# Optimization experiments

Hardware: AMD Instinct MI355X
Metric: run time of the kernel (lower is better)

The kernel has to match this reference:

```python
import jax, jax.numpy as jnp
import numpy as np

B, N, T, H = 64, 16, 128, 256  # batch, max_neighbors, time_steps, hidden_dim


def setup_inputs() -> dict:
    key = jax.random.key(0)
    ks = jax.random.split(key, 7)
    inv_h = 1.0 / np.sqrt(H)
    return {
        "node_rnn_output": jax.random.normal(ks[0], (B, T, H), jnp.float32),
        "neigh_rnn_output": jax.random.normal(ks[1], (B, N, T, H), jnp.float32),
        "neighbors_number": N,
        "Wq": jax.random.normal(ks[2], (H, H), jnp.float32) * inv_h,
        "Wk": jax.random.normal(ks[3], (H, H), jnp.float32) * inv_h,
        "Wv": jax.random.normal(ks[4], (H, H), jnp.float32) * inv_h,
        "Wb": jax.random.normal(ks[5], (H, H), jnp.float32) * inv_h,
        "b": jnp.zeros((T,), jnp.float32),
    }


def reference(node_rnn_output, neigh_rnn_output, neighbors_number, Wq, Wk, Wv, Wb, b):
    # key_values: node prepended to neighbors -> [B, N+1, T, H]
    kv = jnp.concatenate((node_rnn_output[:, None], neigh_rnn_output), axis=1)
    # torch nn.Linear: x @ W^T
    q = node_rnn_output @ Wq.T            # [B, T, H] (query is identical across neighbor slots)
    key = kv @ Wk.T                       # [B, N+1, T, H]
    value = kv @ Wv.T                     # [B, N+1, T, H]
    # bilinear score: (q @ Wb) @ key^T + b  (b broadcasts over last axis)
    qW = q @ Wb                           # [B, T, H]
    S = jnp.einsum('bth,bnsh->bnts', qW, key) + b  # [B, N+1, T, T]
    A = jax.nn.softmax(S, axis=-1)        # dropout is identity at eval / drop_prob=0
    outputs = jnp.einsum('bnts,bnsh->bnth', A, value)  # [B, N+1, T, H]
    return outputs, A
```

## Files before the change

### kernel.cpp

```cpp
#include <hip/hip_runtime.h>
#include <cstdio>


typedef __bf16 bf16;
typedef __attribute__((ext_vector_type(8))) __bf16 bf16x8;
typedef __attribute__((ext_vector_type(4))) __bf16 bf16x4;
typedef __attribute__((ext_vector_type(4))) float floatx4;

#define MFMA_BF16 __builtin_amdgcn_mfma_f32_16x16x32_bf16

__device__ __forceinline__ const float* kv_row_ptr(const float* node, const float* neigh, int bn, int s) {
  int b = bn / 17, nn = bn % 17;
  return (nn == 0) ? node + ((size_t)b * 128 + s) * 256
                   : neigh + (((size_t)b * 16 + (nn - 1)) * 128 + s) * 256;
}

__global__ __launch_bounds__(256) void k_wc(const float* __restrict__ Wq, const float* __restrict__ Wb,
                                            float* __restrict__ Wc) {
  int m = blockIdx.x, h = threadIdx.x;
  float acc = 0.f;
  for (int k = 0; k < 256; ++k) acc = fmaf(Wq[k * 256 + m], Wb[k * 256 + h], acc);
  Wc[m * 256 + h] = acc;
}

__global__ __launch_bounds__(256) void k_we(const float* __restrict__ Wc, const float* __restrict__ Wk,
                                            float* __restrict__ We) {
  int m = blockIdx.x, g = threadIdx.x;
  float acc = 0.f;
  for (int k = 0; k < 256; ++k) acc = fmaf(Wc[m * 256 + k], Wk[k * 256 + g], acc);
  We[m * 256 + g] = acc;
}

__global__ __launch_bounds__(256) void k_wvb(const float* __restrict__ Wv, bf16* __restrict__ Wvb) {
  int i = (blockIdx.x * 256 + threadIdx.x) * 4;
  float4 v = *(const float4*)(Wv + i);
  bf16x4 o;
  o[0] = (bf16)v.x; o[1] = (bf16)v.y; o[2] = (bf16)v.z; o[3] = (bf16)v.w;
  *(bf16x4*)(Wvb + i) = o;
}

__global__ __launch_bounds__(256) void k_qwk(const float* __restrict__ X, const float* __restrict__ W,
                                             float* __restrict__ Y) {
  __shared__ float As[32][64];
  __shared__ float Bs[32][64];
  int tid = threadIdx.x;
  int m0 = blockIdx.x * 64, n0 = blockIdx.y * 64;
  int tx = tid & 15, ty = tid >> 4;
  float acc[4][4] = {};
  int r = tid >> 3, c4 = (tid & 7) * 4;
  int kr = tid >> 4, c4b = (tid & 15) * 4;
  for (int k0 = 0; k0 < 256; k0 += 32) {
#pragma unroll
    for (int p = 0; p < 2; ++p) {
      float4 v = *(const float4*)(X + (size_t)(m0 + r + p * 32) * 256 + k0 + c4);
      As[c4 + 0][r + p * 32] = v.x; As[c4 + 1][r + p * 32] = v.y;
      As[c4 + 2][r + p * 32] = v.z; As[c4 + 3][r + p * 32] = v.w;
    }
#pragma unroll
    for (int p = 0; p < 2; ++p) {
      float4 v = *(const float4*)(W + (size_t)(k0 + kr + p * 16) * 256 + n0 + c4b);
      *(float4*)&Bs[kr + p * 16][c4b] = v;
    }
    __syncthreads();
#pragma unroll 8
    for (int k = 0; k < 32; ++k) {
      float a[4], bb[4];
#pragma unroll
      for (int i = 0; i < 4; ++i) a[i] = As[k][ty * 4 + i];
#pragma unroll
      for (int j = 0; j < 4; ++j) bb[j] = Bs[k][tx * 4 + j];
#pragma unroll
      for (int i = 0; i < 4; ++i)
#pragma unroll
        for (int j = 0; j < 4; ++j) acc[i][j] = fmaf(a[i], bb[j], acc[i][j]);
    }
    __syncthreads();
  }
#pragma unroll
  for (int i = 0; i < 4; ++i) {
    float4 v = make_float4(acc[i][0], acc[i][1], acc[i][2], acc[i][3]);
    *(float4*)(Y + (size_t)(m0 + ty * 4 + i) * 256 + n0 + tx * 4) = v;
  }
}

#define QKS 40
#define ABS 136
__global__ __launch_bounds__(256) void k_fused(const float* __restrict__ qWk, const float* __restrict__ node,
                                               const float* __restrict__ neigh, const float* __restrict__ bvec,
                                               const bf16* __restrict__ Wvb,
                                               float* __restrict__ Aout, float* __restrict__ Out) {
  __shared__ __align__(16) char smem[52224];
  bf16* Khi = (bf16*)smem;
  bf16* Klo = (bf16*)(smem + 10240);
  bf16* Ab  = (bf16*)smem;
  bf16* Vt  = (bf16*)(smem + 34816);

  int tid = threadIdx.x;
  int w = tid >> 6, lane = tid & 63, lrow = lane & 15, quad = lane >> 4;
  int bn = blockIdx.x;
  const float* Q = qWk + (size_t)(bn / 17) * 128 * 256;
  const float* K = kv_row_ptr(node, neigh, bn, 0);

  int srow = tid >> 1;
  int skb = (tid & 1) * 16;

  floatx4 acc[2][8];
#pragma unroll
  for (int rt = 0; rt < 2; ++rt)
#pragma unroll
    for (int ct = 0; ct < 8; ++ct) acc[rt][ct] = (floatx4)0.0f;

  const float* kb = K + (size_t)srow * 256 + skb;
  const float* qlane = Q + (size_t)(w * 32 + lrow) * 256 + quad * 8;
  float4 pk[4];
#pragma unroll
  for (int j = 0; j < 4; ++j) pk[j] = *(const float4*)(kb + j * 4);

  for (int k0 = 0; k0 < 256; k0 += 32) {
#pragma unroll
    for (int half = 0; half < 2; ++half) {
      float kf[8] = {pk[half * 2].x, pk[half * 2].y, pk[half * 2].z, pk[half * 2].w,
                     pk[half * 2 + 1].x, pk[half * 2 + 1].y, pk[half * 2 + 1].z, pk[half * 2 + 1].w};
      bf16x8 kh, kl;
#pragma unroll
      for (int u = 0; u < 8; ++u) {
        bf16 h2 = (bf16)kf[u]; kh[u] = h2; kl[u] = (bf16)(kf[u] - (float)h2);
      }
      int off = srow * QKS + skb + half * 8;
      *(bf16x8*)&Khi[off] = kh; *(bf16x8*)&Klo[off] = kl;
    }
    if (k0 < 224) {
#pragma unroll
      for (int j = 0; j < 4; ++j) pk[j] = *(const float4*)(kb + k0 + 32 + j * 4);
    }
    float4 q0[2], q1[2];
#pragma unroll
    for (int rt = 0; rt < 2; ++rt) {
      const float* qp = qlane + (size_t)rt * 16 * 256 + k0;
      q0[rt] = *(const float4*)qp;
      q1[rt] = *(const float4*)(qp + 4);
    }
    __syncthreads();
    bf16x8 ah[2], al[2];
#pragma unroll
    for (int rt = 0; rt < 2; ++rt) {
      float qf[8] = {q0[rt].x, q0[rt].y, q0[rt].z, q0[rt].w,
                     q1[rt].x, q1[rt].y, q1[rt].z, q1[rt].w};
#pragma unroll
      for (int u = 0; u < 8; ++u) {
        bf16 h = (bf16)qf[u]; ah[rt][u] = h; al[rt][u] = (bf16)(qf[u] - (float)h);
      }
    }
#pragma unroll
    for (int ct = 0; ct < 8; ++ct) {
      int off = (ct * 16 + lrow) * QKS + quad * 8;
      bf16x8 bh = *(const bf16x8*)&Khi[off];
      bf16x8 bl = *(const bf16x8*)&Klo[off];
#pragma unroll
      for (int rt = 0; rt < 2; ++rt) {
        acc[rt][ct] = MFMA_BF16(ah[rt], bh, acc[rt][ct], 0, 0, 0);
        acc[rt][ct] = MFMA_BF16(al[rt], bh, acc[rt][ct], 0, 0, 0);
        acc[rt][ct] = MFMA_BF16(ah[rt], bl, acc[rt][ct], 0, 0, 0);
      }
    }
    __syncthreads();
  }

  float bvv[8];
#pragma unroll
  for (int ct = 0; ct < 8; ++ct) bvv[ct] = bvec[ct * 16 + lrow];
#pragma unroll
  for (int rt = 0; rt < 2; ++rt)
#pragma unroll
    for (int r = 0; r < 4; ++r) {
      float mx = -3.402823466e+38f;
#pragma unroll
      for (int ct = 0; ct < 8; ++ct) {
        float v = acc[rt][ct][r] + bvv[ct];
        acc[rt][ct][r] = v;
        mx = fmaxf(mx, v);
      }
#pragma unroll
      for (int off = 1; off < 16; off <<= 1) mx = fmaxf(mx, __shfl_xor(mx, off, 64));
      float s = 0.f;
#pragma unroll
      for (int ct = 0; ct < 8; ++ct) {
        float e = __expf(acc[rt][ct][r] - mx);
        acc[rt][ct][r] = e;
        s += e;
      }
#pragma unroll
      for (int off = 1; off < 16; off <<= 1) s += __shfl_xor(s, off, 64);
      float inv = 1.f / s;
#pragma unroll
      for (int ct = 0; ct < 8; ++ct) acc[rt][ct][r] *= inv;
    }

  float* Ag = Aout + (size_t)bn * 128 * 128;
#pragma unroll
  for (int rt = 0; rt < 2; ++rt)
#pragma unroll
    for (int r = 0; r < 4; ++r) {
      int row = w * 32 + rt * 16 + quad * 4 + r;
#pragma unroll
      for (int ct = 0; ct < 8; ++ct) {
        int s = ct * 16 + lrow;
        float v = acc[rt][ct][r];
        Ag[(size_t)row * 128 + s] = v;
        Ab[row * ABS + s] = (bf16)v;
      }
    }

  float* Ob = Out + (size_t)bn * 128 * 256;
  for (int hh = 0; hh < 2; ++hh) {
    const int H0 = hh * 128;
    floatx4 vacc[2][8];
#pragma unroll
    for (int rt = 0; rt < 2; ++rt)
#pragma unroll
      for (int ct = 0; ct < 8; ++ct) vacc[rt][ct] = (floatx4)0.0f;

#pragma unroll
    for (int kk = 0; kk < 8; ++kk) {
      bf16x8 af[2];
#pragma unroll
      for (int rt = 0; rt < 2; ++rt) {
        const float* kp = K + (size_t)(w * 32 + rt * 16 + lrow) * 256 + kk * 32 + quad * 8;
        float4 a = *(const float4*)kp, b2 = *(const float4*)(kp + 4);
        bf16x8 o;
        o[0] = (bf16)a.x;  o[1] = (bf16)a.y;  o[2] = (bf16)a.z;  o[3] = (bf16)a.w;
        o[4] = (bf16)b2.x; o[5] = (bf16)b2.y; o[6] = (bf16)b2.z; o[7] = (bf16)b2.w;
        af[rt] = o;
      }
#pragma unroll
      for (int ct = 0; ct < 8; ++ct) {
        bf16x8 bwv = *(const bf16x8*)&Wvb[(size_t)(H0 + ct * 16 + lrow) * 256 + kk * 32 + quad * 8];
#pragma unroll
        for (int rt = 0; rt < 2; ++rt)
          vacc[rt][ct] = MFMA_BF16(af[rt], bwv, vacc[rt][ct], 0, 0, 0);
      }
    }

#pragma unroll
    for (int hc = 0; hc < 2; ++hc) {
#pragma unroll
      for (int ct = 0; ct < 4; ++ct)
#pragma unroll
        for (int rt = 0; rt < 2; ++rt) {
          bf16x4 o;
#pragma unroll
          for (int r = 0; r < 4; ++r) o[r] = (bf16)vacc[rt][hc * 4 + ct][r];
          *(bf16x4*)&Vt[(ct * 16 + lrow) * ABS + w * 32 + rt * 16 + quad * 4] = o;
        }
      __syncthreads();
      floatx4 pacc[2][4];
#pragma unroll
      for (int rt = 0; rt < 2; ++rt)
#pragma unroll
        for (int ct = 0; ct < 4; ++ct) pacc[rt][ct] = (floatx4)0.0f;
#pragma unroll
      for (int s0 = 0; s0 < 128; s0 += 32) {
        bf16x8 paf[2];
#pragma unroll
        for (int rt = 0; rt < 2; ++rt)
          paf[rt] = *(const bf16x8*)&Ab[(w * 32 + rt * 16 + lrow) * ABS + s0 + quad * 8];
#pragma unroll
        for (int ct = 0; ct < 4; ++ct) {
          bf16x8 bv8 = *(const bf16x8*)&Vt[(ct * 16 + lrow) * ABS + s0 + quad * 8];
#pragma unroll
          for (int rt = 0; rt < 2; ++rt)
            pacc[rt][ct] = MFMA_BF16(paf[rt], bv8, pacc[rt][ct], 0, 0, 0);
        }
      }
#pragma unroll
      for (int rt = 0; rt < 2; ++rt)
#pragma unroll
        for (int ct = 0; ct < 4; ++ct)
#pragma unroll
          for (int r = 0; r < 4; ++r) {
            int row = w * 32 + rt * 16 + quad * 4 + r;
            Ob[(size_t)row * 256 + H0 + hc * 64 + ct * 16 + lrow] = pacc[rt][ct][r];
          }
      __syncthreads();
    }
  }
}

extern "C" void kernel_launch(void* const* d_in, const int* in_sizes, int n_in,
                              void* d_out, int out_size, void* d_ws, size_t ws_size,
                              hipStream_t stream) {
  const float* node  = (const float*)d_in[0];
  const float* neigh = (const float*)d_in[1];
  const float* Wq = (const float*)d_in[3];
  const float* Wk = (const float*)d_in[4];
  const float* Wv = (const float*)d_in[5];
  const float* Wb = (const float*)d_in[6];
  const float* bv = (const float*)d_in[7];

  float* out  = (float*)d_out;
  float* Aout = out + (size_t)64 * 17 * 128 * 256;

  size_t need = (size_t)(65536 + 65536 + 2097152) * 4 + (size_t)65536 * 2;
  if (ws_size < need) { fprintf(stderr, "ws too small: %zu < %zu\n", ws_size, need); return; }
  float* wsf = (float*)d_ws;
  float* Wc  = wsf;
  float* We  = wsf + 65536;
  float* qWk = wsf + 131072;
  bf16*  Wvb = (bf16*)(wsf + 131072 + 2097152);

  k_wvb<<<64, 256, 0, stream>>>(Wv, Wvb);
  k_wc<<<256, 256, 0, stream>>>(Wq, Wb, Wc);
  k_we<<<256, 256, 0, stream>>>(Wc, Wk, We);
  k_qwk<<<dim3(128, 4), 256, 0, stream>>>(node, We, qWk);
  k_fused<<<1088, 256, 0, stream>>>(qWk, node, neigh, bv, Wvb, Aout, out);
}
```

Baseline: 495.0 us.

## Use 512-thread blocks in fused attention and tile weight-combination GEMMs

New measurement: 604.2 us. 1.22x slower.

```diff
diff --git a/kernel.cpp b/kernel.cpp
--- a/kernel.cpp
+++ b/kernel.cpp
@@ -13,22 +13,6 @@
   int b = bn / 17, nn = bn % 17;
   return (nn == 0) ? node + ((size_t)b * 128 + s) * 256
                    : neigh + (((size_t)b * 16 + (nn - 1)) * 128 + s) * 256;
-}
-
-__global__ __launch_bounds__(256) void k_wc(const float* __restrict__ Wq, const float* __restrict__ Wb,
-                                            float* __restrict__ Wc) {
-  int m = blockIdx.x, h = threadIdx.x;
-  float acc = 0.f;
-  for (int k = 0; k < 256; ++k) acc = fmaf(Wq[k * 256 + m], Wb[k * 256 + h], acc);
-  Wc[m * 256 + h] = acc;
-}
-
-__global__ __launch_bounds__(256) void k_we(const float* __restrict__ Wc, const float* __restrict__ Wk,
-                                            float* __restrict__ We) {
-  int m = blockIdx.x, g = threadIdx.x;
-  float acc = 0.f;
-  for (int k = 0; k < 256; ++k) acc = fmaf(Wc[m * 256 + k], Wk[k * 256 + g], acc);
-  We[m * 256 + g] = acc;
 }
 
 __global__ __launch_bounds__(256) void k_wvb(const float* __restrict__ Wv, bf16* __restrict__ Wvb) {
@@ -37,6 +21,45 @@
   bf16x4 o;
   o[0] = (bf16)v.x; o[1] = (bf16)v.y; o[2] = (bf16)v.z; o[3] = (bf16)v.w;
   *(bf16x4*)(Wvb + i) = o;
+}
+
+__global__ __launch_bounds__(256) void k_atb(const float* __restrict__ A, const float* __restrict__ B,
+                                             float* __restrict__ C) {
+  __shared__ float As[32][64];
+  __shared__ float Bs[32][64];
+  int tid = threadIdx.x;
+  int m0 = blockIdx.x * 64, n0 = blockIdx.y * 64;
+  int tx = tid & 15, ty = tid >> 4;
+  float acc[4][4] = {};
+  int kr = tid >> 4, c4 = (tid & 15) * 4;
+  for (int k0 = 0; k0 < 256; k0 += 32) {
+#pragma unroll
+    for (int p = 0; p < 2; ++p) {
+      float4 va = *(const float4*)(A + (size_t)(k0 + kr + p * 16) * 256 + m0 + c4);
+      *(float4*)&As[kr + p * 16][c4] = va;
+      float4 vb = *(const float4*)(B + (size_t)(k0 + kr + p * 16) * 256 + n0 + c4);
+      *(float4*)&Bs[kr + p * 16][c4] = vb;
+    }
+    __syncthreads();
+#pragma unroll 8
+    for (int k = 0; k < 32; ++k) {
+      float a[4], bb[4];
+#pragma unroll
+      for (int i = 0; i < 4; ++i) a[i] = As[k][ty * 4 + i];
+#pragma unroll
+      for (int j = 0; j < 4; ++j) bb[j] = Bs[k][tx * 4 + j];
+#pragma unroll
+      for (int i = 0; i < 4; ++i)
+#pragma unroll
+        for (int j = 0; j < 4; ++j) acc[i][j] = fmaf(a[i], bb[j], acc[i][j]);
+    }
+    __syncthreads();
+  }
+#pragma unroll
+  for (int i = 0; i < 4; ++i) {
+    float4 v = make_float4(acc[i][0], acc[i][1], acc[i][2], acc[i][3]);
+    *(float4*)(C + (size_t)(m0 + ty * 4 + i) * 256 + n0 + tx * 4) = v;
+  }
 }
 
 __global__ __launch_bounds__(256) void k_qwk(const float* __restrict__ X, const float* __restrict__ W,
@@ -85,10 +108,10 @@
 
 #define QKS 40
 #define ABS 136
-__global__ __launch_bounds__(256) void k_fused(const float* __restrict__ qWk, const float* __restrict__ node,
-                                               const float* __restrict__ neigh, const float* __restrict__ bvec,
-                                               const bf16* __restrict__ Wvb,
-                                               float* __restrict__ Aout, float* __restrict__ Out) {
+__global__ __launch_bounds__(512, 4) void k_fused(const float* __restrict__ qWk, const float* __restrict__ node,
+                                                  const float* __restrict__ neigh, const float* __restrict__ bvec,
+                                                  const bf16* __restrict__ Wvb,
+                                                  float* __restrict__ Aout, float* __restrict__ Out) {
   __shared__ __align__(16) char smem[52224];
   bf16* Khi = (bf16*)smem;
   bf16* Klo = (bf16*)(smem + 10240);
@@ -101,54 +124,43 @@
   const float* Q = qWk + (size_t)(bn / 17) * 128 * 256;
   const float* K = kv_row_ptr(node, neigh, bn, 0);
 
-  int srow = tid >> 1;
-  int skb = (tid & 1) * 16;
-
-  floatx4 acc[2][8];
-#pragma unroll
-  for (int rt = 0; rt < 2; ++rt)
-#pragma unroll
-    for (int ct = 0; ct < 8; ++ct) acc[rt][ct] = (floatx4)0.0f;
+  int srow = tid >> 2;
+  int skb = (tid & 3) * 8;
+
+  floatx4 acc[8];
+#pragma unroll
+  for (int ct = 0; ct < 8; ++ct) acc[ct] = (floatx4)0.0f;
 
   const float* kb = K + (size_t)srow * 256 + skb;
-  const float* qlane = Q + (size_t)(w * 32 + lrow) * 256 + quad * 8;
-  float4 pk[4];
-#pragma unroll
-  for (int j = 0; j < 4; ++j) pk[j] = *(const float4*)(kb + j * 4);
+  const float* qlane = Q + (size_t)(w * 16 + lrow) * 256 + quad * 8;
+  float4 pk[2];
+#pragma unroll
+  for (int j = 0; j < 2; ++j) pk[j] = *(const float4*)(kb + j * 4);
 
   for (int k0 = 0; k0 < 256; k0 += 32) {
-#pragma unroll
-    for (int half = 0; half < 2; ++half) {
-      float kf[8] = {pk[half * 2].x, pk[half * 2].y, pk[half * 2].z, pk[half * 2].w,
-                     pk[half * 2 + 1].x, pk[half * 2 + 1].y, pk[half * 2 + 1].z, pk[half * 2 + 1].w};
+    {
+      float kf[8] = {pk[0].x, pk[0].y, pk[0].z, pk[0].w, pk[1].x, pk[1].y, pk[1].z, pk[1].w};
       bf16x8 kh, kl;
 #pragma unroll
       for (int u = 0; u < 8; ++u) {
         bf16 h2 = (bf16)kf[u]; kh[u] = h2; kl[u] = (bf16)(kf[u] - (float)h2);
       }
-      int off = srow * QKS + skb + half * 8;
+      int off = srow * QKS + skb;
       *(bf16x8*)&Khi[off] = kh; *(bf16x8*)&Klo[off] = kl;
     }
     if (k0 < 224) {
 #pragma unroll
-      for (int j = 0; j < 4; ++j) pk[j] = *(const float4*)(kb + k0 + 32 + j * 4);
-    }
-    float4 q0[2], q1[2];
-#pragma unroll
-    for (int rt = 0; rt < 2; ++rt) {
-      const float* qp = qlane + (size_t)rt * 16 * 256 + k0;
-      q0[rt] = *(const float4*)qp;
-      q1[rt] = *(const float4*)(qp + 4);
-    }
-    __syncthreads();
-    bf16x8 ah[2], al[2];
-#pragma unroll
-    for (int rt = 0; rt < 2; ++rt) {
-      float qf[8] = {q0[rt].x, q0[rt].y, q0[rt].z, q0[rt].w,
-                     q1[rt].x, q1[rt].y, q1[rt].z, q1[rt].w};
+      for (int j = 0; j < 2; ++j) pk[j] = *(const float4*)(kb + k0 + 32 + j * 4);
+    }
+    float4 q0 = *(const float4*)(qlane + k0);
+    float4 q1 = *(const float4*)(qlane + k0 + 4);
+    __syncthreads();
+    bf16x8 ah, al;
+    {
+      float qf[8] = {q0.x, q0.y, q0.z, q0.w, q1.x, q1.y, q1.z, q1.w};
 #pragma unroll
       for (int u = 0; u < 8; ++u) {
-        bf16 h = (bf16)qf[u]; ah[rt][u] = h; al[rt][u] = (bf16)(qf[u] - (float)h);
+        bf16 h = (bf16)qf[u]; ah[u] = h; al[u] = (bf16)(qf[u] - (float)h);
       }
     }
 #pragma unroll
@@ -156,12 +168,9 @@
       int off = (ct * 16 + lrow) * QKS + quad * 8;
       bf16x8 bh = *(const bf16x8*)&Khi[off];
       bf16x8 bl = *(const bf16x8*)&Klo[off];
-#pragma unroll
-      for (int rt = 0; rt < 2; ++rt) {
-        acc[rt][ct] = MFMA_BF16(ah[rt], bh, acc[rt][ct], 0, 0, 0);
-        acc[rt][ct] = MFMA_BF16(al[rt], bh, acc[rt][ct], 0, 0, 0);
-        acc[rt][ct] = MFMA_BF16(ah[rt], bl, acc[rt][ct], 0, 0, 0);
-      }
+      acc[ct] = MFMA_BF16(ah, bh, acc[ct], 0, 0, 0);
+      acc[ct] = MFMA_BF16(al, bh, acc[ct], 0, 0, 0);
+      acc[ct] = MFMA_BF16(ah, bl, acc[ct], 0, 0, 0);
     }
     __syncthreads();
   }
@@ -170,117 +179,95 @@
 #pragma unroll
   for (int ct = 0; ct < 8; ++ct) bvv[ct] = bvec[ct * 16 + lrow];
 #pragma unroll
-  for (int rt = 0; rt < 2; ++rt)
-#pragma unroll
-    for (int r = 0; r < 4; ++r) {
-      float mx = -3.402823466e+38f;
-#pragma unroll
-      for (int ct = 0; ct < 8; ++ct) {
-        float v = acc[rt][ct][r] + bvv[ct];
-        acc[rt][ct][r] = v;
-        mx = fmaxf(mx, v);
-      }
-#pragma unroll
-      for (int off = 1; off < 16; off <<= 1) mx = fmaxf(mx, __shfl_xor(mx, off, 64));
-      float s = 0.f;
-#pragma unroll
-      for (int ct = 0; ct < 8; ++ct) {
-        float e = __expf(acc[rt][ct][r] - mx);
-        acc[rt][ct][r] = e;
-        s += e;
-      }
-#pragma unroll
-      for (int off = 1; off < 16; off <<= 1) s += __shfl_xor(s, off, 64);
-      float inv = 1.f / s;
-#pragma unroll
-      for (int ct = 0; ct < 8; ++ct) acc[rt][ct][r] *= inv;
-    }
+  for (int r = 0; r < 4; ++r) {
+    float mx = -3.402823466e+38f;
+#pragma unroll
+    for (int ct = 0; ct < 8; ++ct) {
+      float v = acc[ct][r] + bvv[ct];
+      acc[ct][r] = v;
+      mx = fmaxf(mx, v);
+    }
+#pragma unroll
+    for (int off = 1; off < 16; off <<= 1) mx = fmaxf(mx, __shfl_xor(mx, off, 64));
+    float s = 0.f;
+#pragma unroll
+    for (int ct = 0; ct < 8; ++ct) {
+      float e = __expf(acc[ct][r] - mx);
+      acc[ct][r] = e;
+      s += e;
+    }
+#pragma unroll
+    for (int off = 1; off < 16; off <<= 1) s += __shfl_xor(s, off, 64);
+    float inv = 1.f / s;
+#pragma unroll
+    for (int ct = 0; ct < 8; ++ct) acc[ct][r] *= inv;
+  }
 
   float* Ag = Aout + (size_t)bn * 128 * 128;
 #pragma unroll
-  for (int rt = 0; rt < 2; ++rt)
-#pragma unroll
-    for (int r = 0; r < 4; ++r) {
-      int row = w * 32 + rt * 16 + quad * 4 + r;
-#pragma unroll
-      for (int ct = 0; ct < 8; ++ct) {
-        int s = ct * 16 + lrow;
-        float v = acc[rt][ct][r];
-        Ag[(size_t)row * 128 + s] = v;
-        Ab[row * ABS + s] = (bf16)v;
-      }
-    }
+  for (int r = 0; r < 4; ++r) {
+    int row = w * 16 + quad * 4 + r;
+#pragma unroll
+    for (int ct = 0; ct < 8; ++ct) {
+      int s = ct * 16 + lrow;
+      float v = acc[ct][r];
+      Ag[(size_t)row * 128 + s] = v;
+      Ab[row * ABS + s] = (bf16)v;
+    }
+  }
 
   float* Ob = Out + (size_t)bn * 128 * 256;
   for (int hh = 0; hh < 2; ++hh) {
     const int H0 = hh * 128;
-    floatx4 vacc[2][8];
-#pragma unroll
-    for (int rt = 0; rt < 2; ++rt)
-#pragma unroll
-      for (int ct = 0; ct < 8; ++ct) vacc[rt][ct] = (floatx4)0.0f;
+    floatx4 vacc[8];
+#pragma unroll
+    for (int ct = 0; ct < 8; ++ct) vacc[ct] = (floatx4)0.0f;
 
 #pragma unroll
     for (int kk = 0; kk < 8; ++kk) {
-      bf16x8 af[2];
-#pragma unroll
-      for (int rt = 0; rt < 2; ++rt) {
-        const float* kp = K + (size_t)(w * 32 + rt * 16 + lrow) * 256 + kk * 32 + quad * 8;
+      bf16x8 af;
+      {
+        const float* kp = K + (size_t)(w * 16 + lrow) * 256 + kk * 32 + quad * 8;
         float4 a = *(const float4*)kp, b2 = *(const float4*)(kp + 4);
-        bf16x8 o;
-        o[0] = (bf16)a.x;  o[1] = (bf16)a.y;  o[2] = (bf16)a.z;  o[3] = (bf16)a.w;
-        o[4] = (bf16)b2.x; o[5] = (bf16)b2.y; o[6] = (bf16)b2.z; o[7] = (bf16)b2.w;
-        af[rt] = o;
+        af[0] = (bf16)a.x;  af[1] = (bf16)a.y;  af[2] = (bf16)a.z;  af[3] = (bf16)a.w;
+        af[4] = (bf16)b2.x; af[5] = (bf16)b2.y; af[6] = (bf16)b2.z; af[7] = (bf16)b2.w;
       }
 #pragma unroll
       for (int ct = 0; ct < 8; ++ct) {
         bf16x8 bwv = *(const bf16x8*)&Wvb[(size_t)(H0 + ct * 16 + lrow) * 256 + kk * 32 + quad * 8];
-#pragma unroll
-        for (int rt = 0; rt < 2; ++rt)
-          vacc[rt][ct] = MFMA_BF16(af[rt], bwv, vacc[rt][ct], 0, 0, 0);
+        vacc[ct] = MFMA_BF16(af, bwv, vacc[ct], 0, 0, 0);
       }
     }
 
 #pragma unroll
     for (int hc = 0; hc < 2; ++hc) {
 #pragma unroll
-      for (int ct = 0; ct < 4; ++ct)
-#pragma unroll
-        for (int rt = 0; rt < 2; ++rt) {
-          bf16x4 o;
-#pragma unroll
-          for (int r = 0; r < 4; ++r) o[r] = (bf16)vacc[rt][hc * 4 + ct][r];
-          *(bf16x4*)&Vt[(ct * 16 + lrow) * ABS + w * 32 + rt * 16 + quad * 4] = o;
-        }
+      for (int ct = 0; ct < 4; ++ct) {
+        bf16x4 o;
+#pragma unroll
+        for (int r = 0; r < 4; ++r) o[r] = (bf16)vacc[hc * 4 + ct][r];
+        *(bf16x4*)&Vt[(ct * 16 + lrow) * ABS + w * 16 + quad * 4] = o;
+      }
       __syncthreads();
-      floatx4 pacc[2][4];
-#pragma unroll
-      for (int rt = 0; rt < 2; ++rt)
-#pragma unroll
-        for (int ct = 0; ct < 4; ++ct) pacc[rt][ct] = (floatx4)0.0f;
+      floatx4 pacc[4];
+#pragma unroll
+      for (int ct = 0; ct < 4; ++ct) pacc[ct] = (floatx4)0.0f;
 #pragma unroll
       for (int s0 = 0; s0 < 128; s0 += 32) {
-        bf16x8 paf[2];
-#pragma unroll
-        for (int rt = 0; rt < 2; ++rt)
-          paf[rt] = *(const bf16x8*)&Ab[(w * 32 + rt * 16 + lrow) * ABS + s0 + quad * 8];
+        bf16x8 paf = *(const bf16x8*)&Ab[(w * 16 + lrow) * ABS + s0 + quad * 8];
 #pragma unroll
         for (int ct = 0; ct < 4; ++ct) {
           bf16x8 bv8 = *(const bf16x8*)&Vt[(ct * 16 + lrow) * ABS + s0 + quad * 8];
-#pragma unroll
-          for (int rt = 0; rt < 2; ++rt)
-            pacc[rt][ct] = MFMA_BF16(paf[rt], bv8, pacc[rt][ct], 0, 0, 0);
+          pacc[ct] = MFMA_BF16(paf, bv8, pacc[ct], 0, 0, 0);
         }
       }
 #pragma unroll
-      for (int rt = 0; rt < 2; ++rt)
-#pragma unroll
-        for (int ct = 0; ct < 4; ++ct)
-#pragma unroll
-          for (int r = 0; r < 4; ++r) {
-            int row = w * 32 + rt * 16 + quad * 4 + r;
-            Ob[(size_t)row * 256 + H0 + hc * 64 + ct * 16 + lrow] = pacc[rt][ct][r];
-          }
+      for (int ct = 0; ct < 4; ++ct)
+#pragma unroll
+        for (int r = 0; r < 4; ++r) {
+          int row = w * 16 + quad * 4 + r;
+          Ob[(size_t)row * 256 + H0 + hc * 64 + ct * 16 + lrow] = pacc[ct][r];
+        }
       __syncthreads();
     }
   }
@@ -309,8 +296,8 @@
   bf16*  Wvb = (bf16*)(wsf + 131072 + 2097152);
 
   k_wvb<<<64, 256, 0, stream>>>(Wv, Wvb);
-  k_wc<<<256, 256, 0, stream>>>(Wq, Wb, Wc);
-  k_we<<<256, 256, 0, stream>>>(Wc, Wk, We);
+  k_atb<<<dim3(4, 4), 256, 0, stream>>>(Wq, Wb, Wc);
+  k_qwk<<<dim3(4, 4), 256, 0, stream>>>(Wc, Wk, We);
   k_qwk<<<dim3(128, 4), 256, 0, stream>>>(node, We, qWk);
-  k_fused<<<1088, 256, 0, stream>>>(qWk, node, neigh, bv, Wvb, Aout, out);
-}
+  k_fused<<<1088, 512, 0, stream>>>(qWk, node, neigh, bv, Wvb, Aout, out);
+}
```
